# Optimization experiments

Measured on AMD Instinct MI355X. Metric: run time of the kernel, lower is better.

Reference implementation:

```python
import jax, jax.numpy as jnp
import numpy as np

E, D, A, F, K = 512, 1024, 128, 32, 31  # encoder_dim, decoder_dim, attention_dim, location_filters, kernel
B, T = 128, 512


def setup_inputs() -> dict:
    key = jax.random.key(0)
    ks = jax.random.split(key, 9)
    s = lambda *sh: 1.0 / np.sqrt(sh[-1])
    return {
        "encoder_outputs": jax.random.normal(ks[0], (B, T, E), jnp.float32),
        "decoder_state": jax.random.normal(ks[1], (B, D), jnp.float32),
        "prev_attention_weights": jax.random.uniform(ks[2], (B, T), jnp.float32),
        # parameters (torch Linear stores [out, in]; Conv1d [out, in, K])
        "W_enc": jax.random.normal(ks[3], (A, E), jnp.float32) * s(A, E),
        "W_dec": jax.random.normal(ks[4], (A, D), jnp.float32) * s(A, D),
        "conv_w": jax.random.normal(ks[5], (F, 1, K), jnp.float32) * (1.0 / np.sqrt(K)),
        "W_loc": jax.random.normal(ks[6], (A, F), jnp.float32) * s(A, F),
        "W_e": jax.random.normal(ks[7], (1, A), jnp.float32) * s(1, A),
        "b_e": jax.random.normal(ks[8], (1,), jnp.float32) * 0.01,
    }


def reference(encoder_outputs, decoder_state, prev_attention_weights,
              W_enc, W_dec, conv_w, W_loc, W_e, b_e):
    # encoder projection: [B,T,E] @ [E,A] -> [B,T,A]
    enc_p = jnp.einsum('bte,ae->bta', encoder_outputs, W_enc)
    # decoder projection: [B,D] -> [B,1,A]
    dec_p = jnp.einsum('bd,ad->ba', decoder_state, W_dec)[:, None, :]
    # location conv: [B,1,T] * [F,1,K] -> [B,F,T], 'same' padding
    loc = jax.lax.conv_general_dilated(
        prev_attention_weights[:, None, :], conv_w,
        window_strides=(1,), padding=[((K - 1) // 2, (K - 1) // 2)],
        dimension_numbers=('NCH', 'OIH', 'NCH'))
    # [B,F,T] -> [B,T,A]
    loc_p = jnp.einsum('bft,af->bta', loc, W_loc)
    # energies: [B,T]
    energies = jnp.einsum('bta,a->bt', jnp.tanh(enc_p + dec_p + loc_p), W_e[0]) + b_e[0]
    attention_weights = jax.nn.softmax(energies, axis=1)
    # context: [B,T] x [B,T,E] -> [B,E]
    context_vector = jnp.einsum('bt,bte->be', attention_weights, encoder_outputs)
    return context_vector, attention_weights
```

## Files before the change

### kernel.cpp

```cpp
#include <hip/hip_runtime.h>
#include <hip/hip_bf16.h>
#include <math.h>

namespace {
constexpr int EDIM  = 512;
constexpr int DDIM  = 1024;
constexpr int ADIM  = 128;
constexpr int FDIM  = 32;
constexpr int KW    = 31;
constexpr int BATCH = 128;
constexpr int TDIM  = 512;

constexpr int BM = 64;
constexpr int BK = 64;

typedef __attribute__((ext_vector_type(8))) short short8;
typedef __attribute__((ext_vector_type(4))) float floatx4;

__device__ __forceinline__ float fast_tanh(float x) {
  x = fminf(9.0f, fmaxf(-9.0f, x));
  float e = __expf(2.0f * x);
  return (e - 1.0f) / (e + 1.0f);
}

__device__ __forceinline__ ushort2 pack_bf16(float x, float y) {
  union { __hip_bfloat162 h; ushort2 u; } cv;
  cv.h = __float22bfloat162_rn(make_float2(x, y));
  return cv.u;
}

__device__ __forceinline__ short8 pack8(floatx4 a, floatx4 b) {
  union { ushort2 u[4]; short8 v; } o;
  o.u[0] = pack_bf16(a[0], a[1]); o.u[1] = pack_bf16(a[2], a[3]);
  o.u[2] = pack_bf16(b[0], b[1]); o.u[3] = pack_bf16(b[2], b[3]);
  return o.v;
}

__global__ __launch_bounds__(256)
void dec_proj_kernel(const float* __restrict__ dec,
                     const float* __restrict__ Wdec,
                     float* __restrict__ dec_p) {
  int b = blockIdx.x, az = blockIdx.y;
  int tid = threadIdx.x;
  int al = tid >> 3, seg = tid & 7;
  int a = az * 32 + al;
  const float* dv = dec + (size_t)b * DDIM;
  const float* wv = Wdec + (size_t)a * DDIM;
  float s = 0.f;
  #pragma unroll 8
  for (int it = 0; it < 32; ++it) {
    int d = it * 32 + seg * 4;
    float4 d4 = *(const float4*)(dv + d);
    float4 w4 = *(const float4*)(wv + d);
    s += d4.x * w4.x + d4.y * w4.y + d4.z * w4.z + d4.w * w4.w;
  }
  s += __shfl_xor(s, 1, 64);
  s += __shfl_xor(s, 2, 64);
  s += __shfl_xor(s, 4, 64);
  if (seg == 0) dec_p[b * ADIM + a] = s;
}

__global__ __launch_bounds__(256)
void energies_kernel(const float* __restrict__ enc,
                     const float* __restrict__ Wenc,
                     const float* __restrict__ pa,
                     const float* __restrict__ convw,
                     const float* __restrict__ Wloc,
                     const float* __restrict__ We,
                     const float* __restrict__ be,
                     const float* __restrict__ dec_p,
                     float* __restrict__ energies) {
  __shared__ ushort As[BM * 64];
  __shared__ ushort Bs[ADIM * 64];
  __shared__ float pa_s[96];
  __shared__ float cw_s[FDIM * 33];
  __shared__ float epart[2 * BM];

  const int tid  = threadIdx.x;
  const int b    = blockIdx.y;
  const int t0   = blockIdx.x * BM;
  const int wave = tid >> 6, lane = tid & 63;
  const int wt = wave >> 1, wa = wave & 1;
  const int lc = lane & 15, lq = lane >> 4;
  const int sw = lc & 7;

  if (tid < 96) {
    int gt = t0 - 15 + tid;
    pa_s[tid] = (gt >= 0 && gt < TDIM) ? pa[b * TDIM + gt] : 0.0f;
  }
  for (int id = tid; id < FDIM * KW; id += 256)
    cw_s[(id / KW) * 33 + (id % KW)] = convw[id];

  const float* gA[2]; ushort* lA[2];
  #pragma unroll
  for (int r = 0; r < 2; ++r) {
    int ca = tid + 256 * r;
    int row = ca >> 3, c = ca & 7;
    gA[r] = enc + ((size_t)(b * TDIM + t0 + row)) * EDIM + c * 8;
    lA[r] = As + row * 64 + (c ^ (row & 7)) * 8;
  }
  const float* gB[4]; ushort* lB[4];
  #pragma unroll
  for (int r = 0; r < 4; ++r) {
    int cb = tid + 256 * r;
    int row = cb >> 3, c = cb & 7;
    gB[r] = Wenc + (size_t)row * EDIM + c * 8;
    lB[r] = Bs + row * 64 + (c ^ (row & 7)) * 8;
  }

  floatx4 ra[2][2], rb[4][2];
  #pragma unroll
  for (int r = 0; r < 2; ++r) {
    ra[r][0] = __builtin_nontemporal_load((const floatx4*)gA[r]);
    ra[r][1] = __builtin_nontemporal_load((const floatx4*)gA[r] + 1);
    gA[r] += BK;
  }
  #pragma unroll
  for (int r = 0; r < 4; ++r) {
    rb[r][0] = *(const floatx4*)(gB[r]);
    rb[r][1] = *(const floatx4*)(gB[r] + 4);
    gB[r] += BK;
  }

  short8 wl[2]; ushort* lWl[2];
  #pragma unroll
  for (int r = 0; r < 2; ++r) {
    int cw = tid + 256 * r;
    int row = cw >> 2, c = cw & 3;
    floatx4 w0 = *(const floatx4*)(Wloc + row * FDIM + c * 8);
    floatx4 w1 = *(const floatx4*)(Wloc + row * FDIM + c * 8 + 4);
    wl[r] = pack8(w0, w1);
    lWl[r] = Bs + row * 64 + (c ^ (row & 7)) * 8;
  }

  __syncthreads();

  const int tl = tid >> 2, fg = tid & 3;
  short8 cvo;
  {
    float cv[8];
    #pragma unroll
    for (int n = 0; n < 8; ++n) {
      int f = fg * 8 + n;
      float s = 0.f;
      #pragma unroll
      for (int k = 0; k < KW; ++k) s += pa_s[tl + k] * cw_s[f * 33 + k];
      cv[n] = s;
    }
    cvo = pack8((floatx4){cv[0], cv[1], cv[2], cv[3]},
                (floatx4){cv[4], cv[5], cv[6], cv[7]});
  }

  floatx4 acc[2][4];
  #pragma unroll
  for (int tt = 0; tt < 2; ++tt)
    #pragma unroll
    for (int aT = 0; aT < 4; ++aT)
      acc[tt][aT] = (floatx4){0.f, 0.f, 0.f, 0.f};

  for (int kt = 0; kt < 8; ++kt) {
    if (kt) __syncthreads();
    #pragma unroll
    for (int r = 0; r < 2; ++r) *(short8*)lA[r] = pack8(ra[r][0], ra[r][1]);
    #pragma unroll
    for (int r = 0; r < 4; ++r) *(short8*)lB[r] = pack8(rb[r][0], rb[r][1]);
    __syncthreads();
    if (kt < 7) {
      #pragma unroll
      for (int r = 0; r < 2; ++r) {
        ra[r][0] = __builtin_nontemporal_load((const floatx4*)gA[r]);
        ra[r][1] = __builtin_nontemporal_load((const floatx4*)gA[r] + 1);
        gA[r] += BK;
      }
      #pragma unroll
      for (int r = 0; r < 4; ++r) {
        rb[r][0] = *(const floatx4*)(gB[r]);
        rb[r][1] = *(const floatx4*)(gB[r] + 4);
        gB[r] += BK;
      }
    }
    #pragma unroll
    for (int kk = 0; kk < 2; ++kk) {
      const int cco = ((kk * 4 + lq) ^ sw) * 8;
      short8 af[2], bf[4];
      #pragma unroll
      for (int tt = 0; tt < 2; ++tt)
        af[tt] = *(const short8*)&As[(wt * 32 + tt * 16 + lc) * 64 + cco];
      #pragma unroll
      for (int aT = 0; aT < 4; ++aT)
        bf[aT] = *(const short8*)&Bs[(wa * 64 + aT * 16 + lc) * 64 + cco];
      #pragma unroll
      for (int tt = 0; tt < 2; ++tt)
        #pragma unroll
        for (int aT = 0; aT < 4; ++aT)
          acc[tt][aT] = __builtin_amdgcn_mfma_f32_16x16x32_bf16(
              af[tt], bf[aT], acc[tt][aT], 0, 0, 0);
    }
  }
  __syncthreads();

  *(short8*)&As[tl * 64 + (fg ^ (tl & 7)) * 8] = cvo;
  *(short8*)lWl[0] = wl[0];
  *(short8*)lWl[1] = wl[1];
  __syncthreads();
  {
    const int cco = (lq ^ sw) * 8;
    short8 af[2], bf[4];
    #pragma unroll
    for (int tt = 0; tt < 2; ++tt)
      af[tt] = *(const short8*)&As[(wt * 32 + tt * 16 + lc) * 64 + cco];
    #pragma unroll
    for (int aT = 0; aT < 4; ++aT)
      bf[aT] = *(const short8*)&Bs[(wa * 64 + aT * 16 + lc) * 64 + cco];
    #pragma unroll
    for (int tt = 0; tt < 2; ++tt)
      #pragma unroll
      for (int aT = 0; aT < 4; ++aT)
        acc[tt][aT] = __builtin_amdgcn_mfma_f32_16x16x32_bf16(
            af[tt], bf[aT], acc[tt][aT], 0, 0, 0);
  }

  float dpv[4], wev[4];
  #pragma unroll
  for (int aT = 0; aT < 4; ++aT) {
    int a = wa * 64 + aT * 16 + lc;
    dpv[aT] = dec_p[b * ADIM + a];
    wev[aT] = We[a];
  }
  #pragma unroll
  for (int tt = 0; tt < 2; ++tt) {
    float es[4] = {0.f, 0.f, 0.f, 0.f};
    #pragma unroll
    for (int aT = 0; aT < 4; ++aT)
      #pragma unroll
      for (int i = 0; i < 4; ++i)
        es[i] += fast_tanh(acc[tt][aT][i] + dpv[aT]) * wev[aT];
    #pragma unroll
    for (int m = 1; m < 16; m <<= 1)
      #pragma unroll
      for (int i = 0; i < 4; ++i) es[i] += __shfl_xor(es[i], m, 64);
    if (lc == 0)
      #pragma unroll
      for (int i = 0; i < 4; ++i)
        epart[wa * 64 + wt * 32 + tt * 16 + lq * 4 + i] = es[i];
  }
  __syncthreads();
  if (tid < BM)
    energies[(size_t)b * TDIM + t0 + tid] = epart[tid] + epart[64 + tid] + be[0];
}

__global__ __launch_bounds__(256)
void softmax_context_kernel(const float* __restrict__ enc,
                            const float* __restrict__ energ,
                            float* __restrict__ attn,
                            float* __restrict__ ctx) {
  __shared__ float aw[TDIM];
  __shared__ float redm[4];
  __shared__ float reds[4];
  const int b = blockIdx.y, ex = blockIdx.x, tid = threadIdx.x;
  const float* row = energ + (size_t)b * TDIM;
  float x0 = row[tid], x1 = row[tid + 256];
  float m = fmaxf(x0, x1);
  #pragma unroll
  for (int off = 32; off; off >>= 1) m = fmaxf(m, __shfl_xor(m, off, 64));
  int wid = tid >> 6, lane = tid & 63;
  if (lane == 0) redm[wid] = m;
  __syncthreads();
  m = fmaxf(fmaxf(redm[0], redm[1]), fmaxf(redm[2], redm[3]));
  float e0 = __expf(x0 - m), e1 = __expf(x1 - m);
  float s = e0 + e1;
  #pragma unroll
  for (int off = 32; off; off >>= 1) s += __shfl_xor(s, off, 64);
  if (lane == 0) reds[wid] = s;
  __syncthreads();
  s = reds[0] + reds[1] + reds[2] + reds[3];
  float inv = 1.0f / s;
  float w0 = e0 * inv, w1 = e1 * inv;
  aw[tid] = w0; aw[tid + 256] = w1;
  if (ex == 0) {
    attn[(size_t)b * TDIM + tid] = w0;
    attn[(size_t)b * TDIM + tid + 256] = w1;
  }
  __syncthreads();
  const int e = ex * 256 + tid;
  const float* ep = enc + ((size_t)b * TDIM) * EDIM + e;
  float acc = 0.f;
  #pragma unroll 16
  for (int t = 0; t < TDIM; ++t) acc += aw[t] * ep[(size_t)t * EDIM];
  ctx[(size_t)b * EDIM + e] = acc;
}

__global__ __launch_bounds__(256)
void softmax_context_inplace_kernel(const float* __restrict__ enc,
                                    float* __restrict__ attn,
                                    float* __restrict__ ctx) {
  __shared__ float aw[TDIM];
  __shared__ float redm[4];
  __shared__ float reds[4];
  const int b = blockIdx.y, tid = threadIdx.x;
  float* row = attn + (size_t)b * TDIM;
  float x0 = row[tid], x1 = row[tid + 256];
  float m = fmaxf(x0, x1);
  #pragma unroll
  for (int off = 32; off; off >>= 1) m = fmaxf(m, __shfl_xor(m, off, 64));
  int wid = tid >> 6, lane = tid & 63;
  if (lane == 0) redm[wid] = m;
  __syncthreads();
  m = fmaxf(fmaxf(redm[0], redm[1]), fmaxf(redm[2], redm[3]));
  float e0 = __expf(x0 - m), e1 = __expf(x1 - m);
  float s = e0 + e1;
  #pragma unroll
  for (int off = 32; off; off >>= 1) s += __shfl_xor(s, off, 64);
  if (lane == 0) reds[wid] = s;
  __syncthreads();
  s = reds[0] + reds[1] + reds[2] + reds[3];
  float inv = 1.0f / s;
  float w0 = e0 * inv, w1 = e1 * inv;
  row[tid] = w0; row[tid + 256] = w1;
  aw[tid] = w0; aw[tid + 256] = w1;
  __syncthreads();
  const float* ep = enc + ((size_t)b * TDIM) * EDIM;
  float a0 = 0.f, a1 = 0.f;
  #pragma unroll 8
  for (int t = 0; t < TDIM; ++t) {
    float w = aw[t];
    a0 += w * ep[(size_t)t * EDIM + tid];
    a1 += w * ep[(size_t)t * EDIM + tid + 256];
  }
  ctx[(size_t)b * EDIM + tid] = a0;
  ctx[(size_t)b * EDIM + tid + 256] = a1;
}

}

extern "C" void kernel_launch(void* const* d_in, const int* in_sizes, int n_in,
                              void* d_out, int out_size, void* d_ws, size_t ws_size,
                              hipStream_t stream) {
  const float* enc   = (const float*)d_in[0];
  const float* dec   = (const float*)d_in[1];
  const float* pa    = (const float*)d_in[2];
  const float* Wenc  = (const float*)d_in[3];
  const float* Wdec  = (const float*)d_in[4];
  const float* convw = (const float*)d_in[5];
  const float* Wloc  = (const float*)d_in[6];
  const float* We    = (const float*)d_in[7];
  const float* be    = (const float*)d_in[8];

  float* ctx  = (float*)d_out;
  float* attn = (float*)d_out + BATCH * EDIM;

  float* dec_p = (float*)d_ws;
  float* energ = dec_p + BATCH * ADIM;

  const size_t need = (size_t)(BATCH * ADIM + BATCH * TDIM) * sizeof(float);

  dim3 g1(BATCH, 4);
  dec_proj_kernel<<<g1, 256, 0, stream>>>(dec, Wdec, dec_p);

  dim3 g2(TDIM / BM, BATCH);
  if (ws_size >= need) {
    energies_kernel<<<g2, 256, 0, stream>>>(enc, Wenc, pa, convw, Wloc, We, be,
                                            dec_p, energ);
    dim3 g3(2, BATCH);
    softmax_context_kernel<<<g3, 256, 0, stream>>>(enc, energ, attn, ctx);
  } else {
    energies_kernel<<<g2, 256, 0, stream>>>(enc, Wenc, pa, convw, Wloc, We, be,
                                            dec_p, attn);
    dim3 g3(1, BATCH);
    softmax_context_inplace_kernel<<<g3, 256, 0, stream>>>(enc, attn, ctx);
  }
}
```

Baseline: 283.3 us.

## Restructure energies GEMM with larger T tile and register-fed A, split context reduction

The energies kernel now handles 128 timesteps per block. Each wave streams its encoder rows straight from global memory into registers as MFMA A-fragments with one-step prefetch, and stages W_enc in shared memory in 128-column phases, covering all 128 attention columns per wave. This cuts block count, redundant W_enc reloads and the LDS staging of the activations, at the cost of more registers and a W_enc reload every phase. The softmax/context kernel splits T across two half-blocks with a shared reduction and doubles the grid along E to add parallelism.

```diff
diff --git a/kernel.cpp b/kernel.cpp
--- a/kernel.cpp
+++ b/kernel.cpp
@@ -10,9 +10,6 @@
 constexpr int KW    = 31;
 constexpr int BATCH = 128;
 constexpr int TDIM  = 512;
-
-constexpr int BM = 64;
-constexpr int BK = 64;
 
 typedef __attribute__((ext_vector_type(8))) short short8;
 typedef __attribute__((ext_vector_type(4))) float floatx4;
@@ -69,184 +66,146 @@
                      const float* __restrict__ We,
                      const float* __restrict__ be,
                      const float* __restrict__ dec_p,
-                     float* __restrict__ energies) {
-  __shared__ ushort As[BM * 64];
-  __shared__ ushort Bs[ADIM * 64];
-  __shared__ float pa_s[96];
+                     float* __restrict__ energ) {
+  __shared__ ushort WencS[16384];
+  __shared__ ushort convS[4096];
+  __shared__ float pa_s[160];
   __shared__ float cw_s[FDIM * 33];
-  __shared__ float epart[2 * BM];
 
   const int tid  = threadIdx.x;
   const int b    = blockIdx.y;
-  const int t0   = blockIdx.x * BM;
+  const int t0b  = blockIdx.x * 128;
   const int wave = tid >> 6, lane = tid & 63;
-  const int wt = wave >> 1, wa = wave & 1;
   const int lc = lane & 15, lq = lane >> 4;
   const int sw = lc & 7;
 
-  if (tid < 96) {
-    int gt = t0 - 15 + tid;
-    pa_s[tid] = (gt >= 0 && gt < TDIM) ? pa[b * TDIM + gt] : 0.0f;
+  if (tid < 158) {
+    int gt = t0b - 15 + tid;
+    pa_s[tid] = (gt >= 0 && gt < TDIM) ? pa[b * TDIM + gt] : 0.f;
   }
   for (int id = tid; id < FDIM * KW; id += 256)
     cw_s[(id / KW) * 33 + (id % KW)] = convw[id];
-
-  const float* gA[2]; ushort* lA[2];
-  #pragma unroll
-  for (int r = 0; r < 2; ++r) {
-    int ca = tid + 256 * r;
-    int row = ca >> 3, c = ca & 7;
-    gA[r] = enc + ((size_t)(b * TDIM + t0 + row)) * EDIM + c * 8;
-    lA[r] = As + row * 64 + (c ^ (row & 7)) * 8;
-  }
-  const float* gB[4]; ushort* lB[4];
-  #pragma unroll
-  for (int r = 0; r < 4; ++r) {
-    int cb = tid + 256 * r;
-    int row = cb >> 3, c = cb & 7;
-    gB[r] = Wenc + (size_t)row * EDIM + c * 8;
-    lB[r] = Bs + row * 64 + (c ^ (row & 7)) * 8;
-  }
-
-  floatx4 ra[2][2], rb[4][2];
-  #pragma unroll
-  for (int r = 0; r < 2; ++r) {
-    ra[r][0] = __builtin_nontemporal_load((const floatx4*)gA[r]);
-    ra[r][1] = __builtin_nontemporal_load((const floatx4*)gA[r] + 1);
-    gA[r] += BK;
-  }
-  #pragma unroll
-  for (int r = 0; r < 4; ++r) {
-    rb[r][0] = *(const floatx4*)(gB[r]);
-    rb[r][1] = *(const floatx4*)(gB[r] + 4);
-    gB[r] += BK;
-  }
-
-  short8 wl[2]; ushort* lWl[2];
-  #pragma unroll
-  for (int r = 0; r < 2; ++r) {
-    int cw = tid + 256 * r;
-    int row = cw >> 2, c = cw & 3;
-    floatx4 w0 = *(const floatx4*)(Wloc + row * FDIM + c * 8);
-    floatx4 w1 = *(const floatx4*)(Wloc + row * FDIM + c * 8 + 4);
-    wl[r] = pack8(w0, w1);
-    lWl[r] = Bs + row * 64 + (c ^ (row & 7)) * 8;
-  }
-
-  __syncthreads();
-
-  const int tl = tid >> 2, fg = tid & 3;
-  short8 cvo;
+  __syncthreads();
+
   {
-    float cv[8];
-    #pragma unroll
-    for (int n = 0; n < 8; ++n) {
-      int f = fg * 8 + n;
+    const int tl = tid >> 1, fh = (tid & 1) * 16;
+    float cv[16];
+    #pragma unroll
+    for (int n = 0; n < 16; ++n) {
       float s = 0.f;
       #pragma unroll
-      for (int k = 0; k < KW; ++k) s += pa_s[tl + k] * cw_s[f * 33 + k];
+      for (int k = 0; k < KW; ++k) s += pa_s[tl + k] * cw_s[(fh + n) * 33 + k];
       cv[n] = s;
     }
-    cvo = pack8((floatx4){cv[0], cv[1], cv[2], cv[3]},
-                (floatx4){cv[4], cv[5], cv[6], cv[7]});
-  }
-
-  floatx4 acc[2][4];
-  #pragma unroll
-  for (int tt = 0; tt < 2; ++tt)
-    #pragma unroll
-    for (int aT = 0; aT < 4; ++aT)
-      acc[tt][aT] = (floatx4){0.f, 0.f, 0.f, 0.f};
-
-  for (int kt = 0; kt < 8; ++kt) {
-    if (kt) __syncthreads();
-    #pragma unroll
-    for (int r = 0; r < 2; ++r) *(short8*)lA[r] = pack8(ra[r][0], ra[r][1]);
-    #pragma unroll
-    for (int r = 0; r < 4; ++r) *(short8*)lB[r] = pack8(rb[r][0], rb[r][1]);
-    __syncthreads();
-    if (kt < 7) {
-      #pragma unroll
-      for (int r = 0; r < 2; ++r) {
-        ra[r][0] = __builtin_nontemporal_load((const floatx4*)gA[r]);
-        ra[r][1] = __builtin_nontemporal_load((const floatx4*)gA[r] + 1);
-        gA[r] += BK;
-      }
-      #pragma unroll
-      for (int r = 0; r < 4; ++r) {
-        rb[r][0] = *(const floatx4*)(gB[r]);
-        rb[r][1] = *(const floatx4*)(gB[r] + 4);
-        gB[r] += BK;
-      }
-    }
-    #pragma unroll
-    for (int kk = 0; kk < 2; ++kk) {
-      const int cco = ((kk * 4 + lq) ^ sw) * 8;
-      short8 af[2], bf[4];
-      #pragma unroll
-      for (int tt = 0; tt < 2; ++tt)
-        af[tt] = *(const short8*)&As[(wt * 32 + tt * 16 + lc) * 64 + cco];
-      #pragma unroll
-      for (int aT = 0; aT < 4; ++aT)
-        bf[aT] = *(const short8*)&Bs[(wa * 64 + aT * 16 + lc) * 64 + cco];
-      #pragma unroll
-      for (int tt = 0; tt < 2; ++tt)
-        #pragma unroll
-        for (int aT = 0; aT < 4; ++aT)
-          acc[tt][aT] = __builtin_amdgcn_mfma_f32_16x16x32_bf16(
-              af[tt], bf[aT], acc[tt][aT], 0, 0, 0);
-    }
-  }
-  __syncthreads();
-
-  *(short8*)&As[tl * 64 + (fg ^ (tl & 7)) * 8] = cvo;
-  *(short8*)lWl[0] = wl[0];
-  *(short8*)lWl[1] = wl[1];
-  __syncthreads();
-  {
-    const int cco = (lq ^ sw) * 8;
-    short8 af[2], bf[4];
-    #pragma unroll
-    for (int tt = 0; tt < 2; ++tt)
-      af[tt] = *(const short8*)&As[(wt * 32 + tt * 16 + lc) * 64 + cco];
-    #pragma unroll
-    for (int aT = 0; aT < 4; ++aT)
-      bf[aT] = *(const short8*)&Bs[(wa * 64 + aT * 16 + lc) * 64 + cco];
-    #pragma unroll
-    for (int tt = 0; tt < 2; ++tt)
-      #pragma unroll
-      for (int aT = 0; aT < 4; ++aT)
-        acc[tt][aT] = __builtin_amdgcn_mfma_f32_16x16x32_bf16(
-            af[tt], bf[aT], acc[tt][aT], 0, 0, 0);
-  }
-
-  float dpv[4], wev[4];
-  #pragma unroll
-  for (int aT = 0; aT < 4; ++aT) {
-    int a = wa * 64 + aT * 16 + lc;
+    union { ushort2 u[8]; short8 v[2]; } o;
+    #pragma unroll
+    for (int n = 0; n < 8; ++n) o.u[n] = pack_bf16(cv[2 * n], cv[2 * n + 1]);
+    *(short8*)&convS[tl * 32 + fh] = o.v[0];
+    *(short8*)&convS[tl * 32 + fh + 8] = o.v[1];
+  }
+
+  #pragma unroll
+  for (int r = 0; r < 8; ++r) {
+    int idx = tid + r * 256;
+    int sup = idx >> 10, i2 = idx & 1023;
+    int row = i2 >> 3, gc = (i2 & 7) ^ (row & 7);
+    const float* g = Wenc + (size_t)row * EDIM + sup * 64 + gc * 8;
+    *(short8*)&WencS[sup * 8192 + i2 * 8] =
+        pack8(*(const floatx4*)g, *(const floatx4*)(g + 4));
+  }
+
+  const float* pA0 = enc + ((size_t)(b * TDIM + t0b + wave * 32 + lc)) * EDIM + lq * 8;
+  const float* pA1 = pA0 + 16 * EDIM;
+  floatx4 c0a = *(const floatx4*)pA0, c0b = *(const floatx4*)(pA0 + 4);
+  floatx4 c1a = *(const floatx4*)pA1, c1b = *(const floatx4*)(pA1 + 4);
+
+  float dpv[8], wev[8];
+  #pragma unroll
+  for (int aT = 0; aT < 8; ++aT) {
+    int a = aT * 16 + lc;
     dpv[aT] = dec_p[b * ADIM + a];
     wev[aT] = We[a];
   }
-  #pragma unroll
-  for (int tt = 0; tt < 2; ++tt) {
+
+  floatx4 acc0[8], acc1[8];
+  #pragma unroll
+  for (int aT = 0; aT < 8; ++aT) {
+    acc0[aT] = (floatx4){0.f, 0.f, 0.f, 0.f};
+    acc1[aT] = (floatx4){0.f, 0.f, 0.f, 0.f};
+  }
+
+  __syncthreads();
+
+  for (int ph = 0; ph < 4; ++ph) {
+    if (ph) {
+      __syncthreads();
+      #pragma unroll
+      for (int r = 0; r < 8; ++r) {
+        int idx = tid + r * 256;
+        int sup = idx >> 10, i2 = idx & 1023;
+        int row = i2 >> 3, gc = (i2 & 7) ^ (row & 7);
+        const float* g = Wenc + (size_t)row * EDIM + ph * 128 + sup * 64 + gc * 8;
+        *(short8*)&WencS[sup * 8192 + i2 * 8] =
+            pack8(*(const floatx4*)g, *(const floatx4*)(g + 4));
+      }
+      __syncthreads();
+    }
+    #pragma unroll
+    for (int st = 0; st < 4; ++st) {
+      const int step = ph * 4 + st;
+      floatx4 n0a = {0,0,0,0}, n0b = {0,0,0,0}, n1a = {0,0,0,0}, n1b = {0,0,0,0};
+      if (step < 15) {
+        const float* q0 = pA0 + (step + 1) * 32;
+        const float* q1 = pA1 + (step + 1) * 32;
+        n0a = *(const floatx4*)q0; n0b = *(const floatx4*)(q0 + 4);
+        n1a = *(const floatx4*)q1; n1b = *(const floatx4*)(q1 + 4);
+      }
+      short8 af0 = pack8(c0a, c0b);
+      short8 af1 = pack8(c1a, c1b);
+      const int cco = (((st & 1) * 4 + lq) ^ sw) * 8;
+      const ushort* Bb = &WencS[(st >> 1) * 8192 + cco];
+      #pragma unroll
+      for (int aT = 0; aT < 8; ++aT) {
+        short8 bf = *(const short8*)&Bb[(aT * 16 + lc) * 64];
+        acc0[aT] = __builtin_amdgcn_mfma_f32_16x16x32_bf16(af0, bf, acc0[aT], 0, 0, 0);
+        acc1[aT] = __builtin_amdgcn_mfma_f32_16x16x32_bf16(af1, bf, acc1[aT], 0, 0, 0);
+      }
+      c0a = n0a; c0b = n0b; c1a = n1a; c1b = n1b;
+    }
+  }
+
+  {
+    short8 afl0 = *(const short8*)&convS[(wave * 32 + lc) * 32 + lq * 8];
+    short8 afl1 = *(const short8*)&convS[(wave * 32 + 16 + lc) * 32 + lq * 8];
+    #pragma unroll
+    for (int aT = 0; aT < 8; ++aT) {
+      const float* g = Wloc + (size_t)(aT * 16 + lc) * FDIM + lq * 8;
+      short8 bfl = pack8(*(const floatx4*)g, *(const floatx4*)(g + 4));
+      acc0[aT] = __builtin_amdgcn_mfma_f32_16x16x32_bf16(afl0, bfl, acc0[aT], 0, 0, 0);
+      acc1[aT] = __builtin_amdgcn_mfma_f32_16x16x32_bf16(afl1, bfl, acc1[aT], 0, 0, 0);
+    }
+  }
+
+  const float be0 = be[0];
+  #pragma unroll
+  for (int s = 0; s < 2; ++s) {
     float es[4] = {0.f, 0.f, 0.f, 0.f};
     #pragma unroll
-    for (int aT = 0; aT < 4; ++aT)
+    for (int aT = 0; aT < 8; ++aT) {
+      const floatx4 av = s ? acc1[aT] : acc0[aT];
       #pragma unroll
       for (int i = 0; i < 4; ++i)
-        es[i] += fast_tanh(acc[tt][aT][i] + dpv[aT]) * wev[aT];
+        es[i] += fast_tanh(av[i] + dpv[aT]) * wev[aT];
+    }
     #pragma unroll
     for (int m = 1; m < 16; m <<= 1)
       #pragma unroll
       for (int i = 0; i < 4; ++i) es[i] += __shfl_xor(es[i], m, 64);
-    if (lc == 0)
-      #pragma unroll
-      for (int i = 0; i < 4; ++i)
-        epart[wa * 64 + wt * 32 + tt * 16 + lq * 4 + i] = es[i];
-  }
-  __syncthreads();
-  if (tid < BM)
-    energies[(size_t)b * TDIM + t0 + tid] = epart[tid] + epart[64 + tid] + be[0];
+    if (lc == 0) {
+      floatx4 ev = {es[0] + be0, es[1] + be0, es[2] + be0, es[3] + be0};
+      *(floatx4*)&energ[(size_t)b * TDIM + t0b + wave * 32 + s * 16 + lq * 4] = ev;
+    }
+  }
 }
 
 __global__ __launch_bounds__(256)
@@ -257,6 +216,7 @@
   __shared__ float aw[TDIM];
   __shared__ float redm[4];
   __shared__ float reds[4];
+  __shared__ float red2[128];
   const int b = blockIdx.y, ex = blockIdx.x, tid = threadIdx.x;
   const float* row = energ + (size_t)b * TDIM;
   float x0 = row[tid], x1 = row[tid + 256];
@@ -282,12 +242,14 @@
     attn[(size_t)b * TDIM + tid + 256] = w1;
   }
   __syncthreads();
-  const int e = ex * 256 + tid;
-  const float* ep = enc + ((size_t)b * TDIM) * EDIM + e;
+  const int j = tid & 127, h = tid >> 7;
+  const float* ep = enc + ((size_t)(b * TDIM + h * 256)) * EDIM + ex * 128 + j;
   float acc = 0.f;
   #pragma unroll 16
-  for (int t = 0; t < TDIM; ++t) acc += aw[t] * ep[(size_t)t * EDIM];
-  ctx[(size_t)b * EDIM + e] = acc;
+  for (int t = 0; t < 256; ++t) acc += aw[h * 256 + t] * ep[(size_t)t * EDIM];
+  if (h == 1) red2[j] = acc;
+  __syncthreads();
+  if (h == 0) ctx[(size_t)b * EDIM + ex * 128 + j] = acc + red2[j];
 }
 
 __global__ __launch_bounds__(256)
@@ -357,11 +319,11 @@
   dim3 g1(BATCH, 4);
   dec_proj_kernel<<<g1, 256, 0, stream>>>(dec, Wdec, dec_p);
 
-  dim3 g2(TDIM / BM, BATCH);
+  dim3 g2(TDIM / 128, BATCH);
   if (ws_size >= need) {
     energies_kernel<<<g2, 256, 0, stream>>>(enc, Wenc, pa, convw, Wloc, We, be,
                                             dec_p, energ);
-    dim3 g3(2, BATCH);
+    dim3 g3(4, BATCH);
     softmax_context_kernel<<<g3, 256, 0, stream>>>(enc, energ, attn, ctx);
   } else {
     energies_kernel<<<g2, 256, 0, stream>>>(enc, Wenc, pa, convw, Wloc, We, be,
```

Measured after the change: 260.8 us. -8.0%, faster.
